# Performance work log

Hardware: AMD Instinct MI355X
Metric: run time of the kernel (lower is better)

Reference implementation:

```python
import jax, jax.numpy as jnp
import numpy as np

K = 2  # number of propagation hops (init kwarg)


def setup_inputs() -> dict:
    key = jax.random.key(0)
    k1, k2, k3, k4 = jax.random.split(key, 4)
    N, E, D_IN, D_OUT = 100000, 1600000, 128, 64
    x = jax.random.normal(k1, (N, D_IN), dtype=jnp.float32)
    edge_index = jax.random.randint(k2, (2, E), 0, N, dtype=jnp.int64)
    W = jax.random.normal(k3, (D_OUT, D_IN), dtype=jnp.float32) * 0.05
    b = jax.random.normal(k4, (D_OUT,), dtype=jnp.float32) * 0.05
    return {"x": x, "edge_index": edge_index, "W": W, "b": b}


def reference(x, edge_index, W, b):
    N = x.shape[0]
    # add self loops
    loop = jnp.arange(N, dtype=edge_index.dtype)
    src = jnp.concatenate([edge_index[0], loop])
    dst = jnp.concatenate([edge_index[1], loop])
    # symmetric GCN normalization: deg over targets, norm = d^-1/2[src]*d^-1/2[dst]
    deg = jax.ops.segment_sum(jnp.ones_like(dst, dtype=x.dtype), dst, num_segments=N)
    dinv = jnp.where(deg > 0, jax.lax.rsqrt(deg), 0.0)
    norm = (dinv[src] * dinv[dst])[:, None]  # [E+N, 1]
    # K-hop propagation: x <- A_hat x
    h = x
    for _ in range(K):
        h = jax.ops.segment_sum(h[src] * norm, dst, num_segments=N)
    emb = h @ W.T + b  # [N, D_OUT]
    out = jax.nn.log_softmax(emb, axis=1)
    return (out, emb)
```

## Files before the change

kernel.cpp:

```cpp
#include <hip/hip_runtime.h>

#define DIN 128
#define DOUT 64
#define SH 8
#define CAP 8192
#define BMAX 512
#define XS_STRIDE (DIN + 4)

typedef unsigned short ushort_t;
typedef float v2f __attribute__((ext_vector_type(2)));

__device__ __forceinline__ ushort_t f2bf(float f) {
    union { float f; unsigned u; } v; v.f = f;
    unsigned r = v.u + 0x7FFF + ((v.u >> 16) & 1);
    return (ushort_t)(r >> 16);
}

__global__ __launch_bounds__(256) void bin_kernel(const int* __restrict__ src,
                                                  const int* __restrict__ dst,
                                                  int* __restrict__ cursor,
                                                  int* __restrict__ binned, int E, int B) {
    __shared__ int hist_s[BMAX], gbase_s[BMAX], cur_s[BMAX];
    for (int i = threadIdx.x; i < B; i += 256) { hist_s[i] = 0; cur_s[i] = 0; }
    __syncthreads();
    int e0 = blockIdx.x * 4096;
    int e1 = min(e0 + 4096, E);
    for (int e = e0 + threadIdx.x; e < e1; e += 256)
        atomicAdd(&hist_s[dst[e] >> SH], 1);
    __syncthreads();
    for (int b = threadIdx.x; b < B; b += 256) {
        int h = hist_s[b];
        gbase_s[b] = h ? atomicAdd(&cursor[b], h) : 0;
    }
    __syncthreads();
    for (int e = e0 + threadIdx.x; e < e1; e += 256) {
        int d = dst[e], s = src[e];
        int b = d >> SH;
        int off  = atomicAdd(&cur_s[b], 1);
        int slot = gbase_s[b] + off;
        if (slot < (b + 1) * CAP)
            binned[slot] = ((d & ((1 << SH) - 1)) << 17) | s;
    }
}

__global__ void init_cursor_kernel(int* cursor, int* csr_pad) {
    int b = blockIdx.x * 256 + threadIdx.x;
    if (b < BMAX) cursor[b] = b * CAP;
    if (b < 64) csr_pad[b] = 0;
}

__global__ __launch_bounds__(256) void csr_kernel(const int* __restrict__ binned,
                                                  const int* __restrict__ cursor,
                                                  int* __restrict__ row_ptr,
                                                  float* __restrict__ dinv,
                                                  int* __restrict__ csr_src, int N) {
    __shared__ int cnt_s[256], off_s[256], bsc[BMAX];
    int b = blockIdx.x;
    int t = threadIdx.x;

    int c0 = cursor[t] - t * CAP;                 if (c0 > CAP) c0 = CAP;
    int c1 = cursor[t + 256] - (t + 256) * CAP;   if (c1 > CAP) c1 = CAP;
    bsc[t] = c0; bsc[t + 256] = c1;
    __syncthreads();
    for (int off = 1; off < BMAX; off <<= 1) {
        int v0 = (t >= off) ? bsc[t - off] : 0;
        int v1 = (t + 256 >= off) ? bsc[t + 256 - off] : 0;
        __syncthreads();
        bsc[t] += v0; bsc[t + 256] += v1;
        __syncthreads();
    }
    int cb = cursor[b] - b * CAP; if (cb > CAP) cb = CAP;
    int base = bsc[b] - cb;
    int ecnt = cb;
    const int* eb = binned + (size_t)b * CAP;

    cnt_s[t] = 0;
    __syncthreads();
    for (int i = t; i < ecnt; i += 256)
        atomicAdd(&cnt_s[eb[i] >> 17], 1);
    __syncthreads();
    int myc = cnt_s[t];
    off_s[t] = myc;
    __syncthreads();
    for (int off = 1; off < 256; off <<= 1) {
        int v = (t >= off) ? off_s[t - off] : 0;
        __syncthreads();
        off_s[t] += v;
        __syncthreads();
    }
    int excl = off_s[t] - myc;
    int node = (b << SH) + t;
    if (node < N) {
        row_ptr[node] = base + excl;
        dinv[node] = rsqrtf((float)myc + 1.0f);
        if (node == N - 1) row_ptr[N] = base + excl + myc;
    }
    __syncthreads();
    off_s[t] = base + excl;
    __syncthreads();
    for (int i = t; i < ecnt; i += 256) {
        int p = eb[i];
        int slot = atomicAdd(&off_s[p >> 17], 1);
        csr_src[slot] = p & 0x1FFFF;
    }
}

__global__ __launch_bounds__(256) void gemm_kernel(const float* __restrict__ x,
                                                   const float* __restrict__ W,
                                                   const float* __restrict__ dinv,
                                                   ushort_t* __restrict__ yb, int N) {
    __shared__ float Ws[DIN * DOUT];
    __shared__ float xs[64 * XS_STRIDE];
    int tid  = threadIdx.x;
    int row0 = blockIdx.x * 64;

    for (int j = tid; j < DIN * DOUT; j += 256)
        Ws[j] = W[(j & 63) * DIN + (j >> 6)];

    for (int j = tid; j < 64 * DIN / 4; j += 256) {
        int r  = j >> 5;
        int c4 = (j & 31) * 4;
        int grow = row0 + r;
        float4 v = {0.f, 0.f, 0.f, 0.f};
        if (grow < N) v = *(const float4*)&x[(size_t)grow * DIN + c4];
        *(float4*)&xs[r * XS_STRIDE + c4] = v;
    }
    __syncthreads();

    int g    = tid & 15;
    int rgl  = (tid >> 4) & 3;
    int wave = tid >> 6;
    int rloc = wave * 16 + rgl * 4;

    float4 acc[4] = {};
    for (int kk = 0; kk < DIN; kk += 4) {
        float4 wv0 = *(const float4*)&Ws[(kk + 0) * DOUT + g * 4];
        float4 wv1 = *(const float4*)&Ws[(kk + 1) * DOUT + g * 4];
        float4 wv2 = *(const float4*)&Ws[(kk + 2) * DOUT + g * 4];
        float4 wv3 = *(const float4*)&Ws[(kk + 3) * DOUT + g * 4];
        #pragma unroll
        for (int r = 0; r < 4; ++r) {
            float4 xv = *(const float4*)&xs[(rloc + r) * XS_STRIDE + kk];
            acc[r].x += xv.x * wv0.x + xv.y * wv1.x + xv.z * wv2.x + xv.w * wv3.x;
            acc[r].y += xv.x * wv0.y + xv.y * wv1.y + xv.z * wv2.y + xv.w * wv3.y;
            acc[r].z += xv.x * wv0.z + xv.y * wv1.z + xv.z * wv2.z + xv.w * wv3.z;
            acc[r].w += xv.x * wv0.w + xv.y * wv1.w + xv.z * wv2.w + xv.w * wv3.w;
        }
    }
    #pragma unroll
    for (int r = 0; r < 4; ++r) {
        int grow = row0 + rloc + r;
        if (grow < N) {
            float dv = dinv[grow];
            ushort4 o;
            o.x = f2bf(acc[r].x * dv); o.y = f2bf(acc[r].y * dv);
            o.z = f2bf(acc[r].z * dv); o.w = f2bf(acc[r].w * dv);
            *(ushort4*)&yb[(size_t)grow * DOUT + g * 4] = o;
        }
    }
}

__device__ __forceinline__ void add_unpack2(v2f* acc, uint4 v) {
    unsigned u[4] = {v.x, v.y, v.z, v.w};
    #pragma unroll
    for (int d = 0; d < 4; ++d) {
        union { unsigned u; float f; } lo, hi;
        lo.u = u[d] << 16;
        hi.u = u[d] & 0xFFFF0000u;
        v2f p; p.x = lo.f; p.y = hi.f;
        acc[d] += p;
    }
}

template <int FINAL>
__global__ __launch_bounds__(256) void gather_kernel(const int* __restrict__ row_ptr,
                                                     const int* __restrict__ csr_src,
                                                     const float* __restrict__ dinv,
                                                     const ushort_t* __restrict__ yin,
                                                     const float* __restrict__ bias,
                                                     ushort_t* __restrict__ yout,
                                                     float* __restrict__ out,
                                                     float* __restrict__ emb, int N) {
    int row = blockIdx.x * 4 + (threadIdx.x >> 6);
    if (row >= N) return;
    int lane = threadIdx.x & 63;
    int fb   = lane & 7;
    int slot = lane >> 3;
    int start = __builtin_amdgcn_readfirstlane(row_ptr[row]);
    int end   = __builtin_amdgcn_readfirstlane(row_ptr[row + 1]);

    const char* ybase = (const char*)yin;
    unsigned fb16 = (unsigned)fb * 16u;

    v2f acc2[4] = {};

    {
        uint4 sv = *(const uint4*)(ybase + (((unsigned)row << 7) + fb16));
        if (slot == 0) add_unpack2(acc2, sv);
    }

    int b = start;
    int nfull = (end - start) >> 3;
    for (int i = 0; i < nfull; ++i, b += 8) {
        int s = csr_src[b + slot];
        uint4 v = *(const uint4*)(ybase + (((unsigned)s << 7) + fb16));
        add_unpack2(acc2, v);
    }
    int rem = end - b;
    if (rem > 0) {
        int ei = b + slot;
        int eidx = (ei < end) ? ei : end - 1;
        int s = csr_src[eidx];
        uint4 v = *(const uint4*)(ybase + (((unsigned)s << 7) + fb16));
        if (slot < rem) add_unpack2(acc2, v);
    }

    float acc[8] = {acc2[0].x, acc2[0].y, acc2[1].x, acc2[1].y,
                    acc2[2].x, acc2[2].y, acc2[3].x, acc2[3].y};

    #pragma unroll
    for (int m = 8; m <= 32; m <<= 1) {
        #pragma unroll
        for (int i = 0; i < 8; ++i) acc[i] += __shfl_xor(acc[i], m, 64);
    }

    float dv = dinv[row];
    if (!FINAL) {
        if (slot == 0) {
            float s2 = dv * dv;
            union { ushort_t us[8]; uint4 u; } o;
            #pragma unroll
            for (int i = 0; i < 8; ++i) o.us[i] = f2bf(acc[i] * s2);
            *(uint4*)(yout + (size_t)row * DOUT + fb * 8) = o.u;
        }
    } else {
        const float4* bp = (const float4*)(bias + fb * 8);
        float4 b0 = bp[0], b1 = bp[1];
        float e[8];
        e[0] = dv * acc[0] + b0.x; e[1] = dv * acc[1] + b0.y;
        e[2] = dv * acc[2] + b0.z; e[3] = dv * acc[3] + b0.w;
        e[4] = dv * acc[4] + b1.x; e[5] = dv * acc[5] + b1.y;
        e[6] = dv * acc[6] + b1.z; e[7] = dv * acc[7] + b1.w;
        float m = e[0];
        #pragma unroll
        for (int i = 1; i < 8; ++i) m = fmaxf(m, e[i]);
        #pragma unroll
        for (int o2 = 1; o2 <= 4; o2 <<= 1) m = fmaxf(m, __shfl_xor(m, o2, 64));
        float ss = 0.f;
        #pragma unroll
        for (int i = 0; i < 8; ++i) ss += expf(e[i] - m);
        #pragma unroll
        for (int o2 = 1; o2 <= 4; o2 <<= 1) ss += __shfl_xor(ss, o2, 64);
        float lg = m + logf(ss);
        if (slot == 0) {
            float4* ep = (float4*)(emb + (size_t)row * DOUT + fb * 8);
            ep[0] = make_float4(e[0], e[1], e[2], e[3]);
            ep[1] = make_float4(e[4], e[5], e[6], e[7]);
            float4* op = (float4*)(out + (size_t)row * DOUT + fb * 8);
            op[0] = make_float4(e[0] - lg, e[1] - lg, e[2] - lg, e[3] - lg);
            op[1] = make_float4(e[4] - lg, e[5] - lg, e[6] - lg, e[7] - lg);
        }
    }
}

extern "C" void kernel_launch(void* const* d_in, const int* in_sizes, int n_in,
                              void* d_out, int out_size, void* d_ws, size_t ws_size,
                              hipStream_t stream) {
    const float* x    = (const float*)d_in[0];
    const int*   edge = (const int*)d_in[1];
    const float* W    = (const float*)d_in[2];
    const float* b    = (const float*)d_in[3];

    const int N = in_sizes[0] / DIN;
    const int E = in_sizes[1] / 2;
    const int* src = edge;
    const int* dst = edge + E;

    float* out_ptr = (float*)d_out;
    float* emb_ptr = out_ptr + (size_t)N * DOUT;

    const int B = (N + (1 << SH) - 1) >> SH;

    int*     cursor      = (int*)d_ws;
    int*     row_ptr     = cursor + BMAX;
    float*   dinv        = (float*)(row_ptr + N + 1);
    int*     csr_src     = (int*)(dinv + N);
    int*     arena       = csr_src + E + 64;
    int*     binned      = arena;
    ushort_t* y0b        = (ushort_t*)arena;
    ushort_t* y1b        = y0b + (size_t)N * DOUT;

    init_cursor_kernel<<<2, 256, 0, stream>>>(cursor, csr_src + E);
    bin_kernel<<<(E + 4095) / 4096, 256, 0, stream>>>(src, dst, cursor, binned, E, B);
    csr_kernel<<<B, 256, 0, stream>>>(binned, cursor, row_ptr, dinv, csr_src, N);

    gemm_kernel<<<(N + 63) / 64, 256, 0, stream>>>(x, W, dinv, y0b, N);

    gather_kernel<0><<<(N + 3) / 4, 256, 0, stream>>>(row_ptr, csr_src, dinv, y0b, b,
                                                      y1b, nullptr, nullptr, N);

    gather_kernel<1><<<(N + 3) / 4, 256, 0, stream>>>(row_ptr, csr_src, dinv, y1b, b,
                                                      nullptr, out_ptr, emb_ptr, N);
}
```

Baseline: 224.4 us.

## Pre-transpose W once and halve GEMM rows per block

The init kernel now writes a transposed copy of W into workspace once. Each GEMM block then fills shared memory with a coalesced float4 copy instead of a strided per-element gather. The GEMM tile also shrinks from 64 to 32 rows per block, with 2 rows per thread, which cuts shared memory per block and raises the block count and possibly occupancy. The cost is that each block now reloads the full 32 KB weight matrix for half as many rows, and each thread does less work per loaded weight.

```diff
diff --git a/kernel.cpp b/kernel.cpp
--- a/kernel.cpp
+++ b/kernel.cpp
@@ -6,6 +6,7 @@
 #define CAP 8192
 #define BMAX 512
 #define XS_STRIDE (DIN + 4)
+#define XROWS 32
 
 typedef unsigned short ushort_t;
 typedef float v2f __attribute__((ext_vector_type(2)));
@@ -43,10 +44,13 @@
     }
 }
 
-__global__ void init_cursor_kernel(int* cursor, int* csr_pad) {
+__global__ void init_cursor_kernel(int* cursor, int* csr_pad,
+                                   const float* __restrict__ W, float* __restrict__ WT) {
     int b = blockIdx.x * 256 + threadIdx.x;
     if (b < BMAX) cursor[b] = b * CAP;
     if (b < 64) csr_pad[b] = 0;
+    for (int j = b; j < DIN * DOUT; j += 2048)
+        WT[j] = W[(j & 63) * DIN + (j >> 6)];
 }
 
 __global__ __launch_bounds__(256) void csr_kernel(const int* __restrict__ binned,
@@ -106,18 +110,20 @@
 }
 
 __global__ __launch_bounds__(256) void gemm_kernel(const float* __restrict__ x,
-                                                   const float* __restrict__ W,
+                                                   const float* __restrict__ WT,
                                                    const float* __restrict__ dinv,
                                                    ushort_t* __restrict__ yb, int N) {
     __shared__ float Ws[DIN * DOUT];
-    __shared__ float xs[64 * XS_STRIDE];
+    __shared__ float xs[XROWS * XS_STRIDE];
     int tid  = threadIdx.x;
-    int row0 = blockIdx.x * 64;
-
-    for (int j = tid; j < DIN * DOUT; j += 256)
-        Ws[j] = W[(j & 63) * DIN + (j >> 6)];
-
-    for (int j = tid; j < 64 * DIN / 4; j += 256) {
+    int row0 = blockIdx.x * XROWS;
+
+    {
+        const float4* s4 = (const float4*)WT;
+        float4* d4 = (float4*)Ws;
+        for (int j = tid; j < DIN * DOUT / 4; j += 256) d4[j] = s4[j];
+    }
+    for (int j = tid; j < XROWS * DIN / 4; j += 256) {
         int r  = j >> 5;
         int c4 = (j & 31) * 4;
         int grow = row0 + r;
@@ -127,34 +133,36 @@
     }
     __syncthreads();
 
-    int g    = tid & 15;
-    int rgl  = (tid >> 4) & 3;
-    int wave = tid >> 6;
-    int rloc = wave * 16 + rgl * 4;
-
-    float4 acc[4] = {};
+    int g  = tid & 15;
+    int rg = tid >> 4;
+    int r0 = rg * 2;
+
+    float4 acc0 = {}, acc1 = {};
     for (int kk = 0; kk < DIN; kk += 4) {
         float4 wv0 = *(const float4*)&Ws[(kk + 0) * DOUT + g * 4];
         float4 wv1 = *(const float4*)&Ws[(kk + 1) * DOUT + g * 4];
         float4 wv2 = *(const float4*)&Ws[(kk + 2) * DOUT + g * 4];
         float4 wv3 = *(const float4*)&Ws[(kk + 3) * DOUT + g * 4];
-        #pragma unroll
-        for (int r = 0; r < 4; ++r) {
-            float4 xv = *(const float4*)&xs[(rloc + r) * XS_STRIDE + kk];
-            acc[r].x += xv.x * wv0.x + xv.y * wv1.x + xv.z * wv2.x + xv.w * wv3.x;
-            acc[r].y += xv.x * wv0.y + xv.y * wv1.y + xv.z * wv2.y + xv.w * wv3.y;
-            acc[r].z += xv.x * wv0.z + xv.y * wv1.z + xv.z * wv2.z + xv.w * wv3.z;
-            acc[r].w += xv.x * wv0.w + xv.y * wv1.w + xv.z * wv2.w + xv.w * wv3.w;
-        }
+        float4 xv0 = *(const float4*)&xs[(r0 + 0) * XS_STRIDE + kk];
+        float4 xv1 = *(const float4*)&xs[(r0 + 1) * XS_STRIDE + kk];
+        acc0.x += xv0.x * wv0.x + xv0.y * wv1.x + xv0.z * wv2.x + xv0.w * wv3.x;
+        acc0.y += xv0.x * wv0.y + xv0.y * wv1.y + xv0.z * wv2.y + xv0.w * wv3.y;
+        acc0.z += xv0.x * wv0.z + xv0.y * wv1.z + xv0.z * wv2.z + xv0.w * wv3.z;
+        acc0.w += xv0.x * wv0.w + xv0.y * wv1.w + xv0.z * wv2.w + xv0.w * wv3.w;
+        acc1.x += xv1.x * wv0.x + xv1.y * wv1.x + xv1.z * wv2.x + xv1.w * wv3.x;
+        acc1.y += xv1.x * wv0.y + xv1.y * wv1.y + xv1.z * wv2.y + xv1.w * wv3.y;
+        acc1.z += xv1.x * wv0.z + xv1.y * wv1.z + xv1.z * wv2.z + xv1.w * wv3.z;
+        acc1.w += xv1.x * wv0.w + xv1.y * wv1.w + xv1.z * wv2.w + xv1.w * wv3.w;
     }
     #pragma unroll
-    for (int r = 0; r < 4; ++r) {
-        int grow = row0 + rloc + r;
+    for (int r = 0; r < 2; ++r) {
+        int grow = row0 + r0 + r;
         if (grow < N) {
             float dv = dinv[grow];
+            float4 a = r ? acc1 : acc0;
             ushort4 o;
-            o.x = f2bf(acc[r].x * dv); o.y = f2bf(acc[r].y * dv);
-            o.z = f2bf(acc[r].z * dv); o.w = f2bf(acc[r].w * dv);
+            o.x = f2bf(a.x * dv); o.y = f2bf(a.y * dv);
+            o.z = f2bf(a.z * dv); o.w = f2bf(a.w * dv);
             *(ushort4*)&yb[(size_t)grow * DOUT + g * 4] = o;
         }
     }
@@ -282,7 +290,8 @@
     const int B = (N + (1 << SH) - 1) >> SH;
 
     int*     cursor      = (int*)d_ws;
-    int*     row_ptr     = cursor + BMAX;
+    float*   WT          = (float*)(cursor + BMAX);
+    int*     row_ptr     = (int*)(WT + DIN * DOUT);
     float*   dinv        = (float*)(row_ptr + N + 1);
     int*     csr_src     = (int*)(dinv + N);
     int*     arena       = csr_src + E + 64;
@@ -290,11 +299,11 @@
     ushort_t* y0b        = (ushort_t*)arena;
     ushort_t* y1b        = y0b + (size_t)N * DOUT;
 
-    init_cursor_kernel<<<2, 256, 0, stream>>>(cursor, csr_src + E);
+    init_cursor_kernel<<<8, 256, 0, stream>>>(cursor, csr_src + E, W, WT);
     bin_kernel<<<(E + 4095) / 4096, 256, 0, stream>>>(src, dst, cursor, binned, E, B);
     csr_kernel<<<B, 256, 0, stream>>>(binned, cursor, row_ptr, dinv, csr_src, N);
 
-    gemm_kernel<<<(N + 63) / 64, 256, 0, stream>>>(x, W, dinv, y0b, N);
+    gemm_kernel<<<(N + XROWS - 1) / XROWS, 256, 0, stream>>>(x, WT, dinv, y0b, N);
 
     gather_kernel<0><<<(N + 3) / 4, 256, 0, stream>>>(row_ptr, csr_src, dinv, y0b, b,
                                                       y1b, nullptr, nullptr, N);
```

After: 203.4 us. 9.3% less time.
